# Optimization experiments

Measured on AMD Instinct MI355X. Metric: run time of the kernel, lower is better.

Reference implementation:

```python
import jax, jax.numpy as jnp
import numpy as np

NUM_CLASSES = 1000
FEAT_DIM = 512
BATCH = 16384


def setup_inputs() -> dict:
    key = jax.random.key(0)
    k1, k2, k3 = jax.random.split(key, 3)
    x = jax.random.normal(k1, (BATCH, FEAT_DIM), dtype=jnp.float32)
    labels = jax.random.randint(k2, (BATCH,), 0, NUM_CLASSES, dtype=jnp.int64)
    centers = jax.random.normal(k3, (NUM_CLASSES, FEAT_DIM), dtype=jnp.float32)
    margin = jnp.ones((1,), dtype=jnp.float32)
    return {"x": x, "labels": labels, "centers": centers, "margin": margin}


def reference(x, labels, centers, margin):
    # squared euclidean distances: [B, C]
    distmat = (
        jnp.sum(x * x, axis=1, keepdims=True)
        + jnp.sum(centers * centers, axis=1)[None, :]
        - 2.0 * (x @ centers.T)
    )
    B, C = distmat.shape
    onehot = labels[:, None] == jnp.arange(C, dtype=labels.dtype)[None, :]  # [B, C]
    # distance to the true-class center
    dist = jnp.sum(jnp.where(onehot, distmat, 0.0), axis=1)  # [B]
    # min distance over all other classes (mask true class with +inf)
    dist_min = jnp.min(jnp.where(onehot, jnp.inf, distmat), axis=1)  # [B]
    m = margin[0]
    loss = jnp.sum(jnp.maximum(m + dist - dist_min, 0.0)) / B
    return loss
```

## Files before the change

### kernel.cpp

```cpp
#include <hip/hip_runtime.h>
#include <hip/hip_bf16.h>

#define BATCH 16384
#define NCLS  1000
#define NPAD  1024
#define FDIM  512

#define CBLK_STRIDE 266240
#define TAIL_OFF    262144
#define XBLK_STRIDE 262144

typedef __bf16 bf16x8 __attribute__((ext_vector_type(8)));
typedef float  f32x16 __attribute__((ext_vector_type(16)));

#define GLOBAL_AS __attribute__((address_space(1)))
#define LDS_AS    __attribute__((address_space(3)))

#define VMCNT(n) asm volatile("s_waitcnt vmcnt(" #n ")" ::: "memory")
#define LGKM0()  asm volatile("s_waitcnt lgkmcnt(0)" ::: "memory")
#define SCHED0() __builtin_amdgcn_sched_barrier(0)
#define BAR()    do { LGKM0(); __builtin_amdgcn_s_barrier(); SCHED0(); } while (0)

__global__ __launch_bounds__(256) void prep(
    const float* __restrict__ centers, const float* __restrict__ x,
    char* __restrict__ cbt, char* __restrict__ xbt, float* __restrict__ out)
{
    const int bid = blockIdx.x, t = threadIdx.x;
    if (bid == 0 && t == 0) out[0] = 0.f;

    if (bid < 256) {
        const int lane = t & 63;
        const int c = bid * 4 + (t >> 6);
        const int cblk = c >> 8, cl = c & 255;
        char* base = cbt + (size_t)cblk * CBLK_STRIDE;

        float4 f0 = make_float4(0.f, 0.f, 0.f, 0.f);
        float4 f1 = make_float4(0.f, 0.f, 0.f, 0.f);
        if (c < NCLS) {
            f0 = *(const float4*)(centers + (size_t)c * FDIM + lane * 8);
            f1 = *(const float4*)(centers + (size_t)c * FDIM + lane * 8 + 4);
        }
        bf16x8 b;
        b[0] = (__bf16)f0.x; b[1] = (__bf16)f0.y; b[2] = (__bf16)f0.z; b[3] = (__bf16)f0.w;
        b[4] = (__bf16)f1.x; b[5] = (__bf16)f1.y; b[6] = (__bf16)f1.z; b[7] = (__bf16)f1.w;
        *(bf16x8*)(base + (lane >> 2) * 16384 + (lane & 3) * 4096 + cl * 16) = b;

        float ssum = f0.x*f0.x + f0.y*f0.y + f0.z*f0.z + f0.w*f0.w
                   + f1.x*f1.x + f1.y*f1.y + f1.z*f1.z + f1.w*f1.w;
        #pragma unroll
        for (int o = 32; o > 0; o >>= 1) ssum += __shfl_down(ssum, o);
        if (lane == 0) {
            const float hf = (c < NCLS) ? (-0.5f * ssum) : -1e30f;
            const __bf16 h = (__bf16)hf;
            const __bf16 l = (c < NCLS) ? (__bf16)(hf - (float)h) : (__bf16)0.f;
            bf16x8 tl;
            #pragma unroll
            for (int e = 0; e < 8; ++e) tl[e] = (__bf16)0.f;
            tl[0] = h; tl[1] = l;
            *(bf16x8*)(base + TAIL_OFF + cl * 16) = tl;
        }
    } else {
        const int pid  = bid - 256;
        const int bblk = pid >> 4, s = pid & 15;
        const float* src = x + (size_t)(bblk * 256 + t) * FDIM + s * 32;
        float4 f[8];
        #pragma unroll
        for (int j = 0; j < 8; ++j) f[j] = *(const float4*)(src + j * 4);
        char* dst = xbt + (size_t)bblk * XBLK_STRIDE + s * 16384 + t * 16;
        #pragma unroll
        for (int c = 0; c < 4; ++c) {
            bf16x8 b;
            b[0] = (__bf16)f[c*2].x;   b[1] = (__bf16)f[c*2].y;
            b[2] = (__bf16)f[c*2].z;   b[3] = (__bf16)f[c*2].w;
            b[4] = (__bf16)f[c*2+1].x; b[5] = (__bf16)f[c*2+1].y;
            b[6] = (__bf16)f[c*2+1].z; b[7] = (__bf16)f[c*2+1].w;
            *(bf16x8*)(dst + c * 4096) = b;
        }
    }
}

__global__ __launch_bounds__(512, 1) void trip_main(
    const int* __restrict__ labels, const char* __restrict__ cbt,
    const char* __restrict__ xbt, float* __restrict__ mxp,
    float* __restrict__ dap)
{
    extern __shared__ char lds[];
    const int t    = threadIdx.x;
    const int lane = t & 63;
    const int w    = t >> 6;
    const int wN   = w & 3, wM = w >> 2;
    const int l31  = lane & 31, hi = lane >> 5;
    const int bid  = blockIdx.x;
    const int cblk = bid >> 6;
    const int bblk = bid & 63;
    const int class0 = cblk * 256;
    const int row0   = bblk * 256;
    const char* cbB  = cbt + (size_t)cblk * CBLK_STRIDE;
    const char* xbB  = xbt + (size_t)bblk * XBLK_STRIDE;

    auto stageA = [&](int ko, int ai) {
        const char* src = cbB + ko * 16384 + t * 16;
        char* dst = lds + ai * 16384 + t * 16;
        __builtin_amdgcn_global_load_lds((const GLOBAL_AS void*)src,
                                         (LDS_AS void*)dst, 16, 0, 0);
        __builtin_amdgcn_global_load_lds((const GLOBAL_AS void*)(src + 8192),
                                         (LDS_AS void*)(dst + 8192), 16, 0, 0);
    };
    auto stageB = [&](int ko, int bi) {
        const char* src = xbB + ko * 16384 + t * 16;
        char* dst = lds + 49152 + bi * 16384 + t * 16;
        __builtin_amdgcn_global_load_lds((const GLOBAL_AS void*)src,
                                         (LDS_AS void*)dst, 16, 0, 0);
        __builtin_amdgcn_global_load_lds((const GLOBAL_AS void*)(src + 8192),
                                         (LDS_AS void*)(dst + 8192), 16, 0, 0);
    };

    f32x16 acc[4][2];
    #pragma unroll
    for (int mi = 0; mi < 4; ++mi)
        #pragma unroll
        for (int ni = 0; ni < 2; ++ni)
            #pragma unroll
            for (int r = 0; r < 16; ++r) acc[mi][ni][r] = 0.f;

    auto compute = [&](int buf) {
        const char* A = lds + buf * 16384;
        const char* B = lds + 49152 + buf * 16384;
        #pragma unroll
        for (int ks = 0; ks < 2; ++ks) {
            const int chunk = ks * 2 + hi;
            bf16x8 a[4], b[2];
            #pragma unroll
            for (int mi = 0; mi < 4; ++mi)
                a[mi] = *(const bf16x8*)(A + chunk * 4096 + (wM * 128 + mi * 32 + l31) * 16);
            #pragma unroll
            for (int ni = 0; ni < 2; ++ni)
                b[ni] = *(const bf16x8*)(B + chunk * 4096 + (wN * 64 + ni * 32 + l31) * 16);
            #pragma unroll
            for (int mi = 0; mi < 4; ++mi)
                #pragma unroll
                for (int ni = 0; ni < 2; ++ni)
                    acc[mi][ni] = __builtin_amdgcn_mfma_f32_32x32x16_bf16(
                        a[mi], b[ni], acc[mi][ni], 0, 0, 0);
        }
    };

    const int lab0 = labels[row0 + wN * 64 + l31];
    const int lab1 = labels[row0 + wN * 64 + 32 + l31];
    SCHED0();
    if (t < 256) {
        const char* src = cbB + TAIL_OFF + t * 16;
        char* dst = lds + 98304 + t * 16;
        __builtin_amdgcn_global_load_lds((const GLOBAL_AS void*)src,
                                         (LDS_AS void*)dst, 16, 0, 0);
    }
    stageA(0, 0); stageB(0, 0);
    SCHED0();
    stageA(1, 1); stageB(1, 1);
    VMCNT(4);
    BAR();

    #pragma unroll
    for (int tt = 0; tt < 16; ++tt) {
        if (tt < 14) {
            const int pre = (tt + 2) % 3;
            stageA(tt + 2, pre);
            stageB(tt + 2, pre);
            VMCNT(4);
        } else if (tt == 14) {
            VMCNT(0);
        }
        compute(tt % 3);
        BAR();
    }

    {
        const char* T = lds + 98304;
        bf16x8 bt;
        #pragma unroll
        for (int e = 0; e < 8; ++e) bt[e] = (__bf16)0.f;
        if (hi == 0) { bt[0] = (__bf16)1.0f; bt[1] = (__bf16)1.0f; }
        #pragma unroll
        for (int mi = 0; mi < 4; ++mi) {
            bf16x8 a = *(const bf16x8*)(T + (wM * 128 + mi * 32 + l31) * 16);
            #pragma unroll
            for (int ni = 0; ni < 2; ++ni)
                acc[mi][ni] = __builtin_amdgcn_mfma_f32_32x32x16_bf16(
                    a, bt, acc[mi][ni], 0, 0, 0);
        }
    }

    const int labBase = class0 + wM * 128 + hi * 4;
    const int labA0 = lab0 - labBase;
    const int labA1 = lab1 - labBase;
    float MX0 = -3e38f, MX1 = -3e38f, DA0 = -3e38f, DA1 = -3e38f;
    #pragma unroll
    for (int mi = 0; mi < 4; ++mi) {
        #pragma unroll
        for (int r = 0; r < 16; ++r) {
            const int pat = mi * 32 + (r & 3) + 8 * (r >> 2);
            {
                const float a = acc[mi][0][r];
                const bool is = (labA0 == pat);
                MX0 = fmaxf(MX0, is ? -3e38f : a);
                DA0 = is ? a : DA0;
            }
            {
                const float a = acc[mi][1][r];
                const bool is = (labA1 == pat);
                MX1 = fmaxf(MX1, is ? -3e38f : a);
                DA1 = is ? a : DA1;
            }
        }
    }
    MX0 = fmaxf(MX0, __shfl_xor(MX0, 32));
    DA0 = fmaxf(DA0, __shfl_xor(DA0, 32));
    MX1 = fmaxf(MX1, __shfl_xor(MX1, 32));
    DA1 = fmaxf(DA1, __shfl_xor(DA1, 32));

    float* sc = (float*)lds;
    const int i0 = (wN * 2 + 0) * 32 + l31;
    const int i1 = (wN * 2 + 1) * 32 + l31;
    if (wM == 1 && hi == 0) {
        sc[i0] = MX0; sc[256 + i0] = DA0;
        sc[i1] = MX1; sc[256 + i1] = DA1;
    }
    __syncthreads();
    if (wM == 0 && hi == 0) {
        const float M0 = fmaxf(MX0, sc[i0]),  D0 = fmaxf(DA0, sc[256 + i0]);
        const float M1 = fmaxf(MX1, sc[i1]),  D1 = fmaxf(DA1, sc[256 + i1]);
        const int rg = row0 + wN * 64 + l31;
        mxp[cblk * BATCH + rg]      = M0;
        dap[cblk * BATCH + rg]      = D0;
        mxp[cblk * BATCH + rg + 32] = M1;
        dap[cblk * BATCH + rg + 32] = D1;
    }
}

__global__ __launch_bounds__(256) void combine(
    const float* __restrict__ mxp, const float* __restrict__ dap,
    const float* __restrict__ margin, float* __restrict__ out)
{
    const int t = threadIdx.x;
    const int row = blockIdx.x * 256 + t;
    float mx = fmaxf(fmaxf(mxp[row], mxp[BATCH + row]),
                     fmaxf(mxp[2 * BATCH + row], mxp[3 * BATCH + row]));
    float da = fmaxf(fmaxf(dap[row], dap[BATCH + row]),
                     fmaxf(dap[2 * BATCH + row], dap[3 * BATCH + row]));
    float loss = fmaxf(margin[0] - 2.f * da + 2.f * mx, 0.f);
    __shared__ float red[4];
    #pragma unroll
    for (int o = 32; o > 0; o >>= 1) loss += __shfl_down(loss, o);
    if ((t & 63) == 0) red[t >> 6] = loss;
    __syncthreads();
    if (t == 0)
        atomicAdd(out, (red[0] + red[1] + red[2] + red[3]) * (1.0f / BATCH));
}

extern "C" void kernel_launch(void* const* d_in, const int* in_sizes, int n_in,
                              void* d_out, int out_size, void* d_ws, size_t ws_size,
                              hipStream_t stream)
{
    const float* x       = (const float*)d_in[0];
    const int*   labels  = (const int*)d_in[1];
    const float* centers = (const float*)d_in[2];
    const float* margin  = (const float*)d_in[3];
    float* out = (float*)d_out;

    char* ws = (char*)d_ws;
    char*  cbt  = ws;
    char*  xbt  = ws + 1064960;
    float* mxp  = (float*)(ws + 17842176);
    float* dap  = (float*)(ws + 18104320);

    (void)hipFuncSetAttribute((const void*)trip_main,
                              hipFuncAttributeMaxDynamicSharedMemorySize, 102400);

    prep<<<1280, 256, 0, stream>>>(centers, x, cbt, xbt, out);
    trip_main<<<256, 512, 102400, stream>>>(labels, cbt, xbt, mxp, dap);
    combine<<<64, 256, 0, stream>>>(mxp, dap, margin, out);
}
```

Measured before the change: 33.55 us.

## Restructure GEMM pipeline into 64-wide K double-buffer with per-chunk interleaved loads

Changes the packed layout so each K stage covers 64 elements (8 chunks of 8), and replaces the triple-buffered 32-wide K loop with a double-buffered 64-wide one. Each stage is split into four sub-steps that prefetch the next stage's slice, fence with barriers, and raise wave priority around the MFMA block. The x-prep kernel now converts 64 floats per thread, using fewer blocks. LDS use grows to about 132 KB and there are more barriers per K step, which may add sync overhead, and the sub-step vmcnt accounting must stay correct.

```diff
diff --git a/kernel.cpp b/kernel.cpp
--- a/kernel.cpp
+++ b/kernel.cpp
@@ -18,8 +18,8 @@
 
 #define VMCNT(n) asm volatile("s_waitcnt vmcnt(" #n ")" ::: "memory")
 #define LGKM0()  asm volatile("s_waitcnt lgkmcnt(0)" ::: "memory")
+#define SBAR()   __builtin_amdgcn_s_barrier()
 #define SCHED0() __builtin_amdgcn_sched_barrier(0)
-#define BAR()    do { LGKM0(); __builtin_amdgcn_s_barrier(); SCHED0(); } while (0)
 
 __global__ __launch_bounds__(256) void prep(
     const float* __restrict__ centers, const float* __restrict__ x,
@@ -43,7 +43,7 @@
         bf16x8 b;
         b[0] = (__bf16)f0.x; b[1] = (__bf16)f0.y; b[2] = (__bf16)f0.z; b[3] = (__bf16)f0.w;
         b[4] = (__bf16)f1.x; b[5] = (__bf16)f1.y; b[6] = (__bf16)f1.z; b[7] = (__bf16)f1.w;
-        *(bf16x8*)(base + (lane >> 2) * 16384 + (lane & 3) * 4096 + cl * 16) = b;
+        *(bf16x8*)(base + (lane >> 3) * 32768 + (lane & 7) * 4096 + cl * 16) = b;
 
         float ssum = f0.x*f0.x + f0.y*f0.y + f0.z*f0.z + f0.w*f0.w
                    + f1.x*f1.x + f1.y*f1.y + f1.z*f1.z + f1.w*f1.w;
@@ -61,14 +61,14 @@
         }
     } else {
         const int pid  = bid - 256;
-        const int bblk = pid >> 4, s = pid & 15;
-        const float* src = x + (size_t)(bblk * 256 + t) * FDIM + s * 32;
-        float4 f[8];
-        #pragma unroll
-        for (int j = 0; j < 8; ++j) f[j] = *(const float4*)(src + j * 4);
-        char* dst = xbt + (size_t)bblk * XBLK_STRIDE + s * 16384 + t * 16;
-        #pragma unroll
-        for (int c = 0; c < 4; ++c) {
+        const int bblk = pid >> 3, s = pid & 7;
+        const float* src = x + (size_t)(bblk * 256 + t) * FDIM + s * 64;
+        float4 f[16];
+        #pragma unroll
+        for (int j = 0; j < 16; ++j) f[j] = *(const float4*)(src + j * 4);
+        char* dst = xbt + (size_t)bblk * XBLK_STRIDE + s * 32768 + t * 16;
+        #pragma unroll
+        for (int c = 0; c < 8; ++c) {
             bf16x8 b;
             b[0] = (__bf16)f[c*2].x;   b[1] = (__bf16)f[c*2].y;
             b[2] = (__bf16)f[c*2].z;   b[3] = (__bf16)f[c*2].w;
@@ -98,21 +98,13 @@
     const char* cbB  = cbt + (size_t)cblk * CBLK_STRIDE;
     const char* xbB  = xbt + (size_t)bblk * XBLK_STRIDE;
 
-    auto stageA = [&](int ko, int ai) {
-        const char* src = cbB + ko * 16384 + t * 16;
-        char* dst = lds + ai * 16384 + t * 16;
-        __builtin_amdgcn_global_load_lds((const GLOBAL_AS void*)src,
-                                         (LDS_AS void*)dst, 16, 0, 0);
-        __builtin_amdgcn_global_load_lds((const GLOBAL_AS void*)(src + 8192),
-                                         (LDS_AS void*)(dst + 8192), 16, 0, 0);
-    };
-    auto stageB = [&](int ko, int bi) {
-        const char* src = xbB + ko * 16384 + t * 16;
-        char* dst = lds + 49152 + bi * 16384 + t * 16;
-        __builtin_amdgcn_global_load_lds((const GLOBAL_AS void*)src,
-                                         (LDS_AS void*)dst, 16, 0, 0);
-        __builtin_amdgcn_global_load_lds((const GLOBAL_AS void*)(src + 8192),
-                                         (LDS_AS void*)(dst + 8192), 16, 0, 0);
+    auto stageU = [&](int T, int u) {
+        const int boff = (T & 1) * 32768 + u * 8192 + t * 16;
+        const int goff = T * 32768 + u * 8192 + t * 16;
+        __builtin_amdgcn_global_load_lds((const GLOBAL_AS void*)(cbB + goff),
+                                         (LDS_AS void*)(lds + boff), 16, 0, 0);
+        __builtin_amdgcn_global_load_lds((const GLOBAL_AS void*)(xbB + goff),
+                                         (LDS_AS void*)(lds + 65536 + boff), 16, 0, 0);
     };
 
     f32x16 acc[4][2];
@@ -122,60 +114,62 @@
         for (int ni = 0; ni < 2; ++ni)
             #pragma unroll
             for (int r = 0; r < 16; ++r) acc[mi][ni][r] = 0.f;
-
-    auto compute = [&](int buf) {
-        const char* A = lds + buf * 16384;
-        const char* B = lds + 49152 + buf * 16384;
-        #pragma unroll
-        for (int ks = 0; ks < 2; ++ks) {
-            const int chunk = ks * 2 + hi;
-            bf16x8 a[4], b[2];
-            #pragma unroll
-            for (int mi = 0; mi < 4; ++mi)
-                a[mi] = *(const bf16x8*)(A + chunk * 4096 + (wM * 128 + mi * 32 + l31) * 16);
-            #pragma unroll
-            for (int ni = 0; ni < 2; ++ni)
-                b[ni] = *(const bf16x8*)(B + chunk * 4096 + (wN * 64 + ni * 32 + l31) * 16);
-            #pragma unroll
-            for (int mi = 0; mi < 4; ++mi)
-                #pragma unroll
-                for (int ni = 0; ni < 2; ++ni)
-                    acc[mi][ni] = __builtin_amdgcn_mfma_f32_32x32x16_bf16(
-                        a[mi], b[ni], acc[mi][ni], 0, 0, 0);
-        }
-    };
 
     const int lab0 = labels[row0 + wN * 64 + l31];
     const int lab1 = labels[row0 + wN * 64 + 32 + l31];
     SCHED0();
     if (t < 256) {
         const char* src = cbB + TAIL_OFF + t * 16;
-        char* dst = lds + 98304 + t * 16;
+        char* dst = lds + 131072 + t * 16;
         __builtin_amdgcn_global_load_lds((const GLOBAL_AS void*)src,
                                          (LDS_AS void*)dst, 16, 0, 0);
     }
-    stageA(0, 0); stageB(0, 0);
     SCHED0();
-    stageA(1, 1); stageB(1, 1);
-    VMCNT(4);
-    BAR();
-
-    #pragma unroll
-    for (int tt = 0; tt < 16; ++tt) {
-        if (tt < 14) {
-            const int pre = (tt + 2) % 3;
-            stageA(tt + 2, pre);
-            stageB(tt + 2, pre);
-            VMCNT(4);
-        } else if (tt == 14) {
-            VMCNT(0);
-        }
-        compute(tt % 3);
-        BAR();
+    stageU(0, 0); SCHED0();
+    stageU(0, 1); SCHED0();
+    stageU(0, 2); SCHED0();
+    stageU(0, 3);
+    VMCNT(6);
+    SBAR(); SCHED0();
+
+    #pragma unroll
+    for (int T = 0; T < 8; ++T) {
+        const char* A = lds + (T & 1) * 32768;
+        const char* B = lds + 65536 + (T & 1) * 32768;
+        #pragma unroll
+        for (int u = 0; u < 4; ++u) {
+            if (T < 7)          VMCNT(4);
+            else if (u == 0)    VMCNT(4);
+            else if (u == 1)    VMCNT(2);
+            else if (u == 2)    VMCNT(0);
+            const int chunk = u * 2 + hi;
+            bf16x8 a0 = *(const bf16x8*)(A + chunk * 4096 + (wM * 128 +  0 + l31) * 16);
+            bf16x8 a1 = *(const bf16x8*)(A + chunk * 4096 + (wM * 128 + 32 + l31) * 16);
+            bf16x8 a2 = *(const bf16x8*)(A + chunk * 4096 + (wM * 128 + 64 + l31) * 16);
+            bf16x8 a3 = *(const bf16x8*)(A + chunk * 4096 + (wM * 128 + 96 + l31) * 16);
+            bf16x8 b0 = *(const bf16x8*)(B + chunk * 4096 + (wN * 64 +  0 + l31) * 16);
+            bf16x8 b1 = *(const bf16x8*)(B + chunk * 4096 + (wN * 64 + 32 + l31) * 16);
+            if (T < 7) stageU(T + 1, u);
+            SBAR();
+            LGKM0();
+            SCHED0();
+            __builtin_amdgcn_s_setprio(1);
+            acc[0][0] = __builtin_amdgcn_mfma_f32_32x32x16_bf16(a0, b0, acc[0][0], 0, 0, 0);
+            acc[0][1] = __builtin_amdgcn_mfma_f32_32x32x16_bf16(a0, b1, acc[0][1], 0, 0, 0);
+            acc[1][0] = __builtin_amdgcn_mfma_f32_32x32x16_bf16(a1, b0, acc[1][0], 0, 0, 0);
+            acc[1][1] = __builtin_amdgcn_mfma_f32_32x32x16_bf16(a1, b1, acc[1][1], 0, 0, 0);
+            acc[2][0] = __builtin_amdgcn_mfma_f32_32x32x16_bf16(a2, b0, acc[2][0], 0, 0, 0);
+            acc[2][1] = __builtin_amdgcn_mfma_f32_32x32x16_bf16(a2, b1, acc[2][1], 0, 0, 0);
+            acc[3][0] = __builtin_amdgcn_mfma_f32_32x32x16_bf16(a3, b0, acc[3][0], 0, 0, 0);
+            acc[3][1] = __builtin_amdgcn_mfma_f32_32x32x16_bf16(a3, b1, acc[3][1], 0, 0, 0);
+            __builtin_amdgcn_s_setprio(0);
+            SBAR();
+            SCHED0();
+        }
     }
 
     {
-        const char* T = lds + 98304;
+        const char* T = lds + 131072;
         bf16x8 bt;
         #pragma unroll
         for (int e = 0; e < 8; ++e) bt[e] = (__bf16)0.f;
@@ -221,6 +215,7 @@
     float* sc = (float*)lds;
     const int i0 = (wN * 2 + 0) * 32 + l31;
     const int i1 = (wN * 2 + 1) * 32 + l31;
+    __syncthreads();
     if (wM == 1 && hi == 0) {
         sc[i0] = MX0; sc[256 + i0] = DA0;
         sc[i1] = MX1; sc[256 + i1] = DA1;
@@ -274,9 +269,9 @@
     float* dap  = (float*)(ws + 18104320);
 
     (void)hipFuncSetAttribute((const void*)trip_main,
-                              hipFuncAttributeMaxDynamicSharedMemorySize, 102400);
-
-    prep<<<1280, 256, 0, stream>>>(centers, x, cbt, xbt, out);
-    trip_main<<<256, 512, 102400, stream>>>(labels, cbt, xbt, mxp, dap);
+                              hipFuncAttributeMaxDynamicSharedMemorySize, 135168);
+
+    prep<<<768, 256, 0, stream>>>(centers, x, cbt, xbt, out);
+    trip_main<<<256, 512, 135168, stream>>>(labels, cbt, xbt, mxp, dap);
     combine<<<64, 256, 0, stream>>>(mxp, dap, margin, out);
 }
```

Result: no change. 33.24 us (-0.9%).

## Halve class tile to 128 and launch 512 blocks for better CU coverage

Applied to the files above, without the earlier changes.

Shrinks the per-block class tile from 256 to 128 classes. This doubles the grid to 512 workgroups on a 256-CU GPU and cuts LDS to about 74KB, with launch bounds raised to allow more waves. The center layout, staging, epilogue indexing and combine kernel (now 8 partials) are adjusted to match. The aim is better occupancy and load balance, at the cost of re-reading x tiles twice as often and a lower MFMA-to-load ratio per block.

```diff
diff --git a/kernel.cpp b/kernel.cpp
--- a/kernel.cpp
+++ b/kernel.cpp
@@ -3,11 +3,10 @@
 
 #define BATCH 16384
 #define NCLS  1000
-#define NPAD  1024
 #define FDIM  512
 
-#define CBLK_STRIDE 266240
-#define TAIL_OFF    262144
+#define CBLK_STRIDE 133120
+#define TAIL_OFF    131072
 #define XBLK_STRIDE 262144
 
 typedef __bf16 bf16x8 __attribute__((ext_vector_type(8)));
@@ -31,7 +30,7 @@
     if (bid < 256) {
         const int lane = t & 63;
         const int c = bid * 4 + (t >> 6);
-        const int cblk = c >> 8, cl = c & 255;
+        const int cblk = c >> 7, cl = c & 127;
         char* base = cbt + (size_t)cblk * CBLK_STRIDE;
 
         float4 f0 = make_float4(0.f, 0.f, 0.f, 0.f);
@@ -43,7 +42,7 @@
         bf16x8 b;
         b[0] = (__bf16)f0.x; b[1] = (__bf16)f0.y; b[2] = (__bf16)f0.z; b[3] = (__bf16)f0.w;
         b[4] = (__bf16)f1.x; b[5] = (__bf16)f1.y; b[6] = (__bf16)f1.z; b[7] = (__bf16)f1.w;
-        *(bf16x8*)(base + (lane >> 2) * 16384 + (lane & 3) * 4096 + cl * 16) = b;
+        *(bf16x8*)(base + (lane >> 2) * 8192 + (lane & 3) * 2048 + cl * 16) = b;
 
         float ssum = f0.x*f0.x + f0.y*f0.y + f0.z*f0.z + f0.w*f0.w
                    + f1.x*f1.x + f1.y*f1.y + f1.z*f1.z + f1.w*f1.w;
@@ -79,7 +78,7 @@
     }
 }
 
-__global__ __launch_bounds__(512, 1) void trip_main(
+__global__ __launch_bounds__(512, 4) void trip_main(
     const int* __restrict__ labels, const char* __restrict__ cbt,
     const char* __restrict__ xbt, float* __restrict__ mxp,
     float* __restrict__ dap)
@@ -93,80 +92,69 @@
     const int bid  = blockIdx.x;
     const int cblk = bid >> 6;
     const int bblk = bid & 63;
-    const int class0 = cblk * 256;
+    const int class0 = cblk * 128;
     const int row0   = bblk * 256;
     const char* cbB  = cbt + (size_t)cblk * CBLK_STRIDE;
     const char* xbB  = xbt + (size_t)bblk * XBLK_STRIDE;
 
-    auto stageA = [&](int ko, int ai) {
-        const char* src = cbB + ko * 16384 + t * 16;
-        char* dst = lds + ai * 16384 + t * 16;
-        __builtin_amdgcn_global_load_lds((const GLOBAL_AS void*)src,
-                                         (LDS_AS void*)dst, 16, 0, 0);
-        __builtin_amdgcn_global_load_lds((const GLOBAL_AS void*)(src + 8192),
-                                         (LDS_AS void*)(dst + 8192), 16, 0, 0);
+    auto stageS = [&](int ko, int buf) {
+        const char* sa = cbB + ko * 8192 + t * 16;
+        __builtin_amdgcn_global_load_lds((const GLOBAL_AS void*)sa,
+            (LDS_AS void*)(lds + buf * 8192 + t * 16), 16, 0, 0);
+        const char* sb = xbB + ko * 16384 + t * 16;
+        char* db = lds + 24576 + buf * 16384 + t * 16;
+        __builtin_amdgcn_global_load_lds((const GLOBAL_AS void*)sb,
+            (LDS_AS void*)db, 16, 0, 0);
+        __builtin_amdgcn_global_load_lds((const GLOBAL_AS void*)(sb + 8192),
+            (LDS_AS void*)(db + 8192), 16, 0, 0);
     };
-    auto stageB = [&](int ko, int bi) {
-        const char* src = xbB + ko * 16384 + t * 16;
-        char* dst = lds + 49152 + bi * 16384 + t * 16;
-        __builtin_amdgcn_global_load_lds((const GLOBAL_AS void*)src,
-                                         (LDS_AS void*)dst, 16, 0, 0);
-        __builtin_amdgcn_global_load_lds((const GLOBAL_AS void*)(src + 8192),
-                                         (LDS_AS void*)(dst + 8192), 16, 0, 0);
-    };
-
-    f32x16 acc[4][2];
-    #pragma unroll
-    for (int mi = 0; mi < 4; ++mi)
+
+    f32x16 acc[2][2];
+    #pragma unroll
+    for (int mi = 0; mi < 2; ++mi)
         #pragma unroll
         for (int ni = 0; ni < 2; ++ni)
             #pragma unroll
             for (int r = 0; r < 16; ++r) acc[mi][ni][r] = 0.f;
 
     auto compute = [&](int buf) {
-        const char* A = lds + buf * 16384;
-        const char* B = lds + 49152 + buf * 16384;
+        const char* A = lds + buf * 8192;
+        const char* B = lds + 24576 + buf * 16384;
         #pragma unroll
         for (int ks = 0; ks < 2; ++ks) {
             const int chunk = ks * 2 + hi;
-            bf16x8 a[4], b[2];
-            #pragma unroll
-            for (int mi = 0; mi < 4; ++mi)
-                a[mi] = *(const bf16x8*)(A + chunk * 4096 + (wM * 128 + mi * 32 + l31) * 16);
-            #pragma unroll
-            for (int ni = 0; ni < 2; ++ni)
-                b[ni] = *(const bf16x8*)(B + chunk * 4096 + (wN * 64 + ni * 32 + l31) * 16);
-            #pragma unroll
-            for (int mi = 0; mi < 4; ++mi)
-                #pragma unroll
-                for (int ni = 0; ni < 2; ++ni)
-                    acc[mi][ni] = __builtin_amdgcn_mfma_f32_32x32x16_bf16(
-                        a[mi], b[ni], acc[mi][ni], 0, 0, 0);
+            bf16x8 a0 = *(const bf16x8*)(A + chunk * 2048 + (wM * 64 +  0 + l31) * 16);
+            bf16x8 a1 = *(const bf16x8*)(A + chunk * 2048 + (wM * 64 + 32 + l31) * 16);
+            bf16x8 b0 = *(const bf16x8*)(B + chunk * 4096 + (wN * 64 +  0 + l31) * 16);
+            bf16x8 b1 = *(const bf16x8*)(B + chunk * 4096 + (wN * 64 + 32 + l31) * 16);
+            acc[0][0] = __builtin_amdgcn_mfma_f32_32x32x16_bf16(a0, b0, acc[0][0], 0, 0, 0);
+            acc[0][1] = __builtin_amdgcn_mfma_f32_32x32x16_bf16(a0, b1, acc[0][1], 0, 0, 0);
+            acc[1][0] = __builtin_amdgcn_mfma_f32_32x32x16_bf16(a1, b0, acc[1][0], 0, 0, 0);
+            acc[1][1] = __builtin_amdgcn_mfma_f32_32x32x16_bf16(a1, b1, acc[1][1], 0, 0, 0);
         }
     };
 
     const int lab0 = labels[row0 + wN * 64 + l31];
     const int lab1 = labels[row0 + wN * 64 + 32 + l31];
     SCHED0();
-    if (t < 256) {
+    if (t < 128) {
         const char* src = cbB + TAIL_OFF + t * 16;
-        char* dst = lds + 98304 + t * 16;
+        char* dst = lds + 73728 + t * 16;
         __builtin_amdgcn_global_load_lds((const GLOBAL_AS void*)src,
                                          (LDS_AS void*)dst, 16, 0, 0);
     }
-    stageA(0, 0); stageB(0, 0);
     SCHED0();
-    stageA(1, 1); stageB(1, 1);
-    VMCNT(4);
+    stageS(0, 0);
+    SCHED0();
+    stageS(1, 1);
+    VMCNT(3);
     BAR();
 
     #pragma unroll
     for (int tt = 0; tt < 16; ++tt) {
         if (tt < 14) {
-            const int pre = (tt + 2) % 3;
-            stageA(tt + 2, pre);
-            stageB(tt + 2, pre);
-            VMCNT(4);
+            stageS(tt + 2, (tt + 2) % 3);
+            VMCNT(3);
         } else if (tt == 14) {
             VMCNT(0);
         }
@@ -175,14 +163,14 @@
     }
 
     {
-        const char* T = lds + 98304;
+        const char* T = lds + 73728;
         bf16x8 bt;
         #pragma unroll
         for (int e = 0; e < 8; ++e) bt[e] = (__bf16)0.f;
         if (hi == 0) { bt[0] = (__bf16)1.0f; bt[1] = (__bf16)1.0f; }
         #pragma unroll
-        for (int mi = 0; mi < 4; ++mi) {
-            bf16x8 a = *(const bf16x8*)(T + (wM * 128 + mi * 32 + l31) * 16);
+        for (int mi = 0; mi < 2; ++mi) {
+            bf16x8 a = *(const bf16x8*)(T + (wM * 64 + mi * 32 + l31) * 16);
             #pragma unroll
             for (int ni = 0; ni < 2; ++ni)
                 acc[mi][ni] = __builtin_amdgcn_mfma_f32_32x32x16_bf16(
@@ -190,12 +178,12 @@
         }
     }
 
-    const int labBase = class0 + wM * 128 + hi * 4;
+    const int labBase = class0 + wM * 64 + hi * 4;
     const int labA0 = lab0 - labBase;
     const int labA1 = lab1 - labBase;
     float MX0 = -3e38f, MX1 = -3e38f, DA0 = -3e38f, DA1 = -3e38f;
     #pragma unroll
-    for (int mi = 0; mi < 4; ++mi) {
+    for (int mi = 0; mi < 2; ++mi) {
         #pragma unroll
         for (int r = 0; r < 16; ++r) {
             const int pat = mi * 32 + (r & 3) + 8 * (r >> 2);
@@ -219,8 +207,8 @@
     DA1 = fmaxf(DA1, __shfl_xor(DA1, 32));
 
     float* sc = (float*)lds;
-    const int i0 = (wN * 2 + 0) * 32 + l31;
-    const int i1 = (wN * 2 + 1) * 32 + l31;
+    const int i0 = wN * 64 + l31;
+    const int i1 = i0 + 32;
     if (wM == 1 && hi == 0) {
         sc[i0] = MX0; sc[256 + i0] = DA0;
         sc[i1] = MX1; sc[256 + i1] = DA1;
@@ -243,10 +231,12 @@
 {
     const int t = threadIdx.x;
     const int row = blockIdx.x * 256 + t;
-    float mx = fmaxf(fmaxf(mxp[row], mxp[BATCH + row]),
-                     fmaxf(mxp[2 * BATCH + row], mxp[3 * BATCH + row]));
-    float da = fmaxf(fmaxf(dap[row], dap[BATCH + row]),
-                     fmaxf(dap[2 * BATCH + row], dap[3 * BATCH + row]));
+    float mx = mxp[row], da = dap[row];
+    #pragma unroll
+    for (int p = 1; p < 8; ++p) {
+        mx = fmaxf(mx, mxp[p * BATCH + row]);
+        da = fmaxf(da, dap[p * BATCH + row]);
+    }
     float loss = fmaxf(margin[0] - 2.f * da + 2.f * mx, 0.f);
     __shared__ float red[4];
     #pragma unroll
@@ -271,12 +261,12 @@
     char*  cbt  = ws;
     char*  xbt  = ws + 1064960;
     float* mxp  = (float*)(ws + 17842176);
-    float* dap  = (float*)(ws + 18104320);
+    float* dap  = (float*)(ws + 18366464);
 
     (void)hipFuncSetAttribute((const void*)trip_main,
-                              hipFuncAttributeMaxDynamicSharedMemorySize, 102400);
+                              hipFuncAttributeMaxDynamicSharedMemorySize, 75776);
 
     prep<<<1280, 256, 0, stream>>>(centers, x, cbt, xbt, out);
-    trip_main<<<256, 512, 102400, stream>>>(labels, cbt, xbt, mxp, dap);
+    trip_main<<<512, 512, 75776, stream>>>(labels, cbt, xbt, mxp, dap);
     combine<<<64, 256, 0, stream>>>(mxp, dap, margin, out);
 }
```

New measurement: 35.07 us. 4.5% more time.
